# Kernel tuning notes

Measured on AMD Instinct MI355X. Metric: run time of the kernel, lower is better.

The kernel has to match this reference:

```python
import jax, jax.numpy as jnp
import numpy as np

NH = 8      # num_head
WIN = 7     # window
EPS = 1e-6


def _ln(x, w, b):
    m = x.mean(-1, keepdims=True)
    v = ((x - m) ** 2).mean(-1, keepdims=True)
    return (x - m) / jnp.sqrt(v + EPS) * w + b


def _dwconv(x, w, b):
    # x: [B,H,W,Cc], w: [7,7,1,Cc] (HWIO), depthwise (groups=Cc)
    y = jax.lax.conv_general_dilated(
        x, w, window_strides=(1, 1), padding='SAME',
        dimension_numbers=('NHWC', 'HWIO', 'NHWC'),
        feature_group_count=x.shape[-1])
    return y + b


def setup_inputs() -> dict:
    B, H, W, C = 16, 56, 56, 256
    RATIO = 8
    key = jax.random.key(0)
    ki = iter(jax.random.split(key, 48))
    def lin(i, o):
        return jax.random.normal(next(ki), (i, o), jnp.float32) * (1.0 / i) ** 0.5
    def bias(o):
        return jnp.zeros((o,), jnp.float32)
    def dw(c):
        return jax.random.normal(next(ki), (7, 7, 1, c), jnp.float32) * 0.05
    inp = {
        'x':   jax.random.normal(next(ki), (B, H, W, C), jnp.float32),
        'x_e': jax.random.normal(next(ki), (B, H, W, C // 2), jnp.float32),
        # LayerNorms
        'norm_w': jnp.ones((C,), jnp.float32),  'norm_b': bias(C),
        'norme_w': jnp.ones((C // 2,), jnp.float32), 'norme_b': bias(C // 2),
        # local_rr path
        'rr1_w': lin(C, C), 'rr1_b': bias(C),
        'rr2_w': lin(C, C), 'rr2_b': bias(C),
        'rr3_w': lin(C, C), 'rr3_b': bias(C),
        'conv_w': dw(C), 'conv_b': bias(C),
        # LocalAttentionRGBT
        'lx_l1_w': lin(C, C // 2), 'lx_l1_b': bias(C // 2),
        'lx_l2_w': lin(C // 2, C // 2), 'lx_l2_b': bias(C // 2),
        'lx_c1_w': dw(C // 2), 'lx_c1_b': bias(C // 2),
        'lx_c2_w': dw(C // 2), 'lx_c2_b': bias(C // 2),
        'lx_fc1_w': lin(C, C // RATIO),  # no bias
        'lx_fc2_w': lin(C // RATIO, C),  # no bias
        'lx_l3_w': lin(C, C // 2), 'lx_l3_b': bias(C // 2),
        # global pooled attention
        'kv_w': lin(C, C), 'kv_b': bias(C),
        'q_w': lin(C // 2 * 3, C // 2), 'q_b': bias(C // 2),
        # output projections (window != 0 => in = 2C)
        'proj_w': lin(2 * C, C), 'proj_b': bias(C),
        'proje_w': lin(2 * C, C // 2), 'proje_b': bias(C // 2),
    }
    return inp


def reference(x, x_e, norm_w, norm_b, norme_w, norme_b,
              rr1_w, rr1_b, rr2_w, rr2_b, rr3_w, rr3_b, conv_w, conv_b,
              lx_l1_w, lx_l1_b, lx_l2_w, lx_l2_b, lx_c1_w, lx_c1_b,
              lx_c2_w, lx_c2_b, lx_fc1_w, lx_fc2_w, lx_l3_w, lx_l3_b,
              kv_w, kv_b, q_w, q_b, proj_w, proj_b, proje_w, proje_b):
    B, H, W, C = x.shape
    hd = C // NH // 2  # head dim
    x = _ln(x, norm_w, norm_b)
    x_e = _ln(x_e, norme_w, norme_b)

    # --- local_rr: gated depthwise-conv branch ---
    rr1 = x @ rr1_w + rr1_b
    rr2 = _dwconv(x @ rr2_w + rr2_b, conv_w, conv_b)
    rr2 = rr2 @ rr3_w + rr3_b
    local_rr = rr1 * rr2  # [B,H,W,C]

    # --- LocalAttentionRGBT: cross-modal cosine-sim channel gate ---
    rgb = x @ lx_l1_w + lx_l1_b      # [B,H,W,C/2]
    t = x_e @ lx_l2_w + lx_l2_b      # [B,H,W,C/2]
    co = _dwconv(rgb * t, lx_c1_w, lx_c1_b)
    di = _dwconv(jnp.abs(rgb - t), lx_c2_w, lx_c2_b)
    co_di = jnp.concatenate([co, di], axis=-1)           # [B,H,W,C]
    amap = co_di.mean(-1, keepdims=True)                 # [B,H,W,1]
    dot = (amap * co_di).sum((1, 2), keepdims=True)      # [B,1,1,C]
    n1 = jnp.sqrt((amap ** 2).sum((1, 2), keepdims=True))
    n2 = jnp.sqrt((co_di ** 2).sum((1, 2), keepdims=True))
    cos_sim = dot / (n1 * n2 + 1e-6)                     # [B,1,1,C]
    attn_c = jax.nn.sigmoid(
        jax.nn.gelu(cos_sim @ lx_fc1_w, approximate=False) @ lx_fc2_w)
    local_rx = (co_di * attn_c) @ lx_l3_w + lx_l3_b      # [B,H,W,C/2]

    # --- global: pooled-q full-kv attention ---
    kv = (x @ kv_w + kv_b).reshape(B, H * W, 2, NH, hd).transpose(2, 0, 3, 1, 4)
    k, v = kv[0], kv[1]                                  # [B,NH,HW,hd]
    rx = jnp.concatenate([x, x_e], axis=-1)              # [B,H,W,3C/2]
    rx_pool = rx.reshape(B, WIN, H // WIN, WIN, W // WIN, -1).mean((2, 4))  # [B,7,7,3C/2]
    q = (rx_pool @ q_w + q_b).reshape(B, WIN * WIN, NH, hd).transpose(0, 2, 1, 3)
    scores = jnp.einsum('bnqd,bnkd->bnqk', q * hd ** -0.5, k)  # [B,NH,49,HW]
    attn = jax.nn.softmax(scores, axis=-1)
    g = jnp.einsum('bnqk,bnkd->bnqd', attn, v)           # [B,NH,49,hd]
    g = g.reshape(B, NH, WIN, WIN, hd).transpose(0, 1, 4, 2, 3).reshape(B, C // 2, WIN, WIN)
    g = jax.image.resize(g, (B, C // 2, H, W), method='bilinear')  # align_corners=False
    g = g.transpose(0, 2, 3, 1)                          # [B,H,W,C/2]

    cat = jnp.concatenate([local_rr, local_rx, g], axis=-1)  # [B,H,W,2C]
    x_e_out = cat @ proje_w + proje_b
    x_out = cat @ proj_w + proj_b
    return (x_out, x_e_out)
```

## Files before the change

### kernel.cpp

```cpp
#include <hip/hip_runtime.h>
#include <hip/hip_bf16.h>
#include <cstdint>
#include <cstddef>

#define N_TOK 50176
#define HWSZ  3136
#define BATCH 16

#define GF_MUL     1
#define GF_ASCALE  2
#define GF_KVSPLIT 4
#define GF_DUAL    8

typedef __hip_bfloat16 bf16;
typedef __attribute__((ext_vector_type(8))) short bf16x8;
typedef __attribute__((ext_vector_type(4))) float f32x4;
typedef __attribute__((ext_vector_type(4))) unsigned short u16x4;

__device__ __forceinline__ void  stf(float* p, size_t i, float v) { p[i] = v; }
__device__ __forceinline__ void  stf(bf16* p, size_t i, float v) { p[i] = __float2bfloat16(v); }
__device__ __forceinline__ float bu2f(unsigned short u) {
    unsigned int x = ((unsigned int)u) << 16; float f; __builtin_memcpy(&f, &x, 4); return f;
}
__device__ __forceinline__ unsigned short f2bu(float f) {
    bf16 t = __float2bfloat16(f); unsigned short u; __builtin_memcpy(&u, &t, 2); return u;
}

struct WtrDesc { const float* src; bf16* dst; int K; int N; int off; };
struct WtrPack { WtrDesc d[9]; int total; };
__global__ __launch_bounds__(256) void wtr_all(WtrPack p)
{
    int idx = blockIdx.x * 256 + threadIdx.x;
    if (idx >= p.total) return;
    #pragma unroll
    for (int s = 0; s < 9; s++) {
        int lo = p.d[s].off, hi = lo + p.d[s].K * p.d[s].N;
        if (idx >= lo && idx < hi) {
            int j = idx - lo;
            int k = j / p.d[s].N, n = j % p.d[s].N;
            p.d[s].dst[(size_t)n * p.d[s].K + k] = __float2bfloat16(p.d[s].src[j]);
        }
    }
}

__global__ __launch_bounds__(256) void ln_kernel(const float* __restrict__ in,
    const float* __restrict__ w, const float* __restrict__ b,
    bf16* __restrict__ out, int rows, int Cdim)
{
    int wave = threadIdx.x >> 6, lane = threadIdx.x & 63;
    int row = blockIdx.x * 4 + wave;
    if (row >= rows) return;
    const float* p = in + (size_t)row * Cdim;
    int nj = Cdim >> 6;
    float v[4];
    float s = 0.f;
    for (int j = 0; j < nj; j++) { v[j] = p[lane + 64 * j]; s += v[j]; }
    for (int off = 32; off; off >>= 1) s += __shfl_xor(s, off, 64);
    float mean = s / (float)Cdim;
    float vs = 0.f;
    for (int j = 0; j < nj; j++) { float d = v[j] - mean; vs += d * d; }
    for (int off = 32; off; off >>= 1) vs += __shfl_xor(vs, off, 64);
    float rstd = 1.f / sqrtf(vs / (float)Cdim + 1e-6f);
    bf16* q = out + (size_t)row * Cdim;
    for (int j = 0; j < nj; j++) {
        int c = lane + 64 * j;
        q[c] = __float2bfloat16((v[j] - mean) * rstd * w[c] + b[c]);
    }
}

#define LDT 40
template<int FLAGS, typename OT>
__global__ __launch_bounds__(256) void gemm_mfma(
    const bf16* __restrict__ A, int lda,
    const bf16* __restrict__ WT,
    const float* __restrict__ bias,
    OT* __restrict__ C, int ldc,
    int M, int K, int N,
    const bf16* __restrict__ mul, int mulld,
    const float* __restrict__ ascale,
    bf16* __restrict__ kout, bf16* __restrict__ vout,
    OT* __restrict__ C2, int ldc2, const float* __restrict__ bias2, int N1)
{
    __shared__ bf16 As[2][64][LDT];
    __shared__ bf16 Bs[2][128][LDT];
    int ntile = N >> 7;
    int bid = blockIdx.x;
    bid = (bid & 7) * (gridDim.x >> 3) + (bid >> 3);
    int m0 = (bid / ntile) * 64;
    int n0 = (bid % ntile) * 128;
    int tid = threadIdx.x;
    int lane = tid & 63, wid = tid >> 6;
    int wc = wid * 32;
    int lrow = lane & 15, lko = (lane >> 4) * 8;
    int sr = tid >> 2, sko = (tid & 3) * 8;

    f32x4 acc[4][2];
    #pragma unroll
    for (int i = 0; i < 4; i++)
        #pragma unroll
        for (int j = 0; j < 2; j++)
            acc[i][j] = (f32x4){0.f, 0.f, 0.f, 0.f};

#define GLOAD(RA, RB0, RB1, KOFF) do {                                                        \
    bf16x8 v_ = *reinterpret_cast<const bf16x8*>(A + (size_t)(m0 + sr) * lda + (KOFF) + sko); \
    if (FLAGS & GF_ASCALE) {                                                                  \
        int bidx_ = (m0 + sr) / HWSZ;                                                         \
        const float* as_ = ascale + (size_t)bidx_ * K + (KOFF) + sko;                         \
        for (int e_ = 0; e_ < 8; e_++)                                                        \
            v_[e_] = (short)f2bu(bu2f((unsigned short)v_[e_]) * as_[e_]);                     \
    }                                                                                         \
    RA = v_;                                                                                  \
    RB0 = *reinterpret_cast<const bf16x8*>(WT + (size_t)(n0 + sr) * K + (KOFF) + sko);        \
    RB1 = *reinterpret_cast<const bf16x8*>(WT + (size_t)(n0 + sr + 64) * K + (KOFF) + sko);   \
} while (0)

#define GWRITE(P, RA, RB0, RB1) do {                                   \
    *reinterpret_cast<bf16x8*>(&As[P][sr][sko]) = RA;                  \
    *reinterpret_cast<bf16x8*>(&Bs[P][sr][sko]) = RB0;                 \
    *reinterpret_cast<bf16x8*>(&Bs[P][sr + 64][sko]) = RB1;            \
} while (0)

#define GCOMP(P) do {                                                                         \
    bf16x8 af_[4], br_[2];                                                                    \
    for (int i_ = 0; i_ < 4; i_++)                                                            \
        af_[i_] = *reinterpret_cast<const bf16x8*>(&As[P][i_ * 16 + lrow][lko]);              \
    for (int j_ = 0; j_ < 2; j_++)                                                            \
        br_[j_] = *reinterpret_cast<const bf16x8*>(&Bs[P][wc + j_ * 16 + lrow][lko]);         \
    for (int i_ = 0; i_ < 4; i_++)                                                            \
        for (int j_ = 0; j_ < 2; j_++)                                                        \
            acc[i_][j_] = __builtin_amdgcn_mfma_f32_16x16x32_bf16(af_[i_], br_[j_], acc[i_][j_], 0, 0, 0); \
} while (0)

    bf16x8 ra0, rb00, rb01, ra1, rb10, rb11;
    GLOAD(ra0, rb00, rb01, 0);
    GLOAD(ra1, rb10, rb11, 32);
    int nst = K >> 5;
    for (int s = 0; s < nst; s += 2) {
        GWRITE(0, ra0, rb00, rb01);
        if (s + 2 < nst) GLOAD(ra0, rb00, rb01, (s + 2) * 32);
        __syncthreads();
        GCOMP(0);
        GWRITE(1, ra1, rb10, rb11);
        if (s + 3 < nst) GLOAD(ra1, rb10, rb11, (s + 3) * 32);
        __syncthreads();
        GCOMP(1);
    }
#undef GLOAD
#undef GWRITE
#undef GCOMP

    int orow = (lane >> 4) * 4;
    int ocol = lane & 15;
    #pragma unroll
    for (int i = 0; i < 4; i++) {
        #pragma unroll
        for (int j = 0; j < 2; j++) {
            #pragma unroll
            for (int p = 0; p < 4; p++) {
                int gm = m0 + i * 16 + orow + p;
                int gn = n0 + wc + j * 16 + ocol;
                if (FLAGS & GF_KVSPLIT) {
                    float v = acc[i][j][p] + bias[gn];
                    int bb = gm / HWSZ, n = gm % HWSZ;
                    if (gn < 128)
                        kout[(((size_t)bb * 8 + (gn >> 4)) * HWSZ + n) * 16 + (gn & 15)] = __float2bfloat16(v);
                    else {
                        int hh = (gn - 128) >> 4, dd = (gn - 128) & 15;
                        vout[(((size_t)bb * 8 + hh) * 16 + dd) * HWSZ + n] = __float2bfloat16(v);
                    }
                } else if (FLAGS & GF_DUAL) {
                    if (gn < N1) {
                        float v = acc[i][j][p] + bias[gn];
                        stf(C, (size_t)gm * ldc + gn, v);
                    } else {
                        float v = acc[i][j][p] + bias2[gn - N1];
                        stf(C2, (size_t)gm * ldc2 + (gn - N1), v);
                    }
                } else {
                    float v = acc[i][j][p] + bias[gn];
                    if (FLAGS & GF_MUL) v *= __bfloat162float(mul[(size_t)gm * mulld + gn]);
                    stf(C, (size_t)gm * ldc + gn, v);
                }
            }
        }
    }
}

__global__ __launch_bounds__(256) void gemm_k(
    const float* __restrict__ A, int lda,
    const float* __restrict__ Wt, const float* __restrict__ bias,
    float* __restrict__ Cc, int ldc, int M, int K, int Nc)
{
    __shared__ float As[16][68];
    __shared__ float Ws[16][64];
    int ntile = Nc >> 6;
    int tile_n = blockIdx.x % ntile;
    int tile_m = blockIdx.x / ntile;
    int m0 = tile_m * 64, n0 = tile_n * 64;
    int tid = threadIdx.x;
    int tx = tid & 15, ty = tid >> 4;
    float acc[4][4] = {};
    for (int k0 = 0; k0 < K; k0 += 16) {
        int ks = tid & 15, ms = tid >> 4;
        #pragma unroll
        for (int i = 0; i < 4; i++) {
            int gm = m0 + ms + i * 16;
            As[ks][ms + i * 16] = (gm < M) ? A[(size_t)gm * lda + k0 + ks] : 0.f;
        }
        #pragma unroll
        for (int j = 0; j < 4; j++) {
            int k = (tid >> 6) * 4 + j;
            Ws[k][tid & 63] = Wt[(size_t)(k0 + k) * Nc + n0 + (tid & 63)];
        }
        __syncthreads();
        #pragma unroll
        for (int k = 0; k < 16; k++) {
            float a[4], w[4];
            #pragma unroll
            for (int i = 0; i < 4; i++) a[i] = As[k][ty * 4 + i];
            #pragma unroll
            for (int j = 0; j < 4; j++) w[j] = Ws[k][tx * 4 + j];
            #pragma unroll
            for (int i = 0; i < 4; i++)
                #pragma unroll
                for (int j = 0; j < 4; j++)
                    acc[i][j] += a[i] * w[j];
        }
        __syncthreads();
    }
    #pragma unroll
    for (int i = 0; i < 4; i++) {
        int gm = m0 + ty * 4 + i;
        if (gm >= M) continue;
        #pragma unroll
        for (int j = 0; j < 4; j++) {
            int gn = n0 + tx * 4 + j;
            Cc[(size_t)gm * ldc + gn] = acc[i][j] + bias[gn];
        }
    }
}

__global__ __launch_bounds__(256) void dwconv_reg(const bf16* __restrict__ in,
    bf16* __restrict__ out,
    const float* __restrict__ w0, const float* __restrict__ b0,
    const float* __restrict__ w1, const float* __restrict__ b1, int split)
{
    int tid = threadIdx.x;
    int chg = tid & 31;
    int bsw = (blockIdx.x & 7) * 196 + (blockIdx.x >> 3);
    int pg  = bsw * 8 + (tid >> 5);
    int xg = pg % 14;
    int y  = (pg / 14) % 56;
    int b  = pg / (14 * 56);
    int c0 = chg * 8;
    int x0 = xg * 4;

    const float* wp; const float* bp; int ws, cw;
    if (c0 < split) { wp = w0; bp = b0; ws = split;       cw = c0; }
    else            { wp = w1; bp = b1; ws = 256 - split; cw = c0 - split; }

    float acc[4][8];
    #pragma unroll
    for (int o = 0; o < 4; o++)
        #pragma unroll
        for (int e = 0; e < 8; e++) acc[o][e] = 0.f;

    const bf16* base = in + (size_t)b * HWSZ * 256 + c0;
    const float* wbase = wp + cw;
    #pragma unroll
    for (int ky = 0; ky < 7; ky++) {
        int gy = y + ky - 3;
        if (gy < 0 || gy >= 56) continue;
        const bf16* rowp = base + (size_t)gy * 56 * 256;
        float cf[10][8];
        #pragma unroll
        for (int j = 0; j < 10; j++) {
            int gx = x0 + j - 3;
            bf16x8 v = {0, 0, 0, 0, 0, 0, 0, 0};
            if ((unsigned)gx < 56u)
                v = *reinterpret_cast<const bf16x8*>(rowp + (size_t)gx * 256);
            #pragma unroll
            for (int e = 0; e < 8; e++) cf[j][e] = bu2f((unsigned short)v[e]);
        }
        const float* wrow = wbase + ky * 7 * ws;
        #pragma unroll
        for (int kx = 0; kx < 7; kx++) {
            float4 wa = *reinterpret_cast<const float4*>(wrow + kx * ws);
            float4 wb = *reinterpret_cast<const float4*>(wrow + kx * ws + 4);
            #pragma unroll
            for (int o = 0; o < 4; o++) {
                acc[o][0] += cf[o + kx][0] * wa.x;
                acc[o][1] += cf[o + kx][1] * wa.y;
                acc[o][2] += cf[o + kx][2] * wa.z;
                acc[o][3] += cf[o + kx][3] * wa.w;
                acc[o][4] += cf[o + kx][4] * wb.x;
                acc[o][5] += cf[o + kx][5] * wb.y;
                acc[o][6] += cf[o + kx][6] * wb.z;
                acc[o][7] += cf[o + kx][7] * wb.w;
            }
        }
    }

    float4 ba = *reinterpret_cast<const float4*>(bp + cw);
    float4 bb = *reinterpret_cast<const float4*>(bp + cw + 4);
    bf16* obase = out + (((size_t)b * HWSZ + (size_t)y * 56 + x0) * 256) + c0;
    #pragma unroll
    for (int o = 0; o < 4; o++) {
        bf16x8 ov;
        ov[0] = (short)f2bu(acc[o][0] + ba.x);
        ov[1] = (short)f2bu(acc[o][1] + ba.y);
        ov[2] = (short)f2bu(acc[o][2] + ba.z);
        ov[3] = (short)f2bu(acc[o][3] + ba.w);
        ov[4] = (short)f2bu(acc[o][4] + bb.x);
        ov[5] = (short)f2bu(acc[o][5] + bb.y);
        ov[6] = (short)f2bu(acc[o][6] + bb.z);
        ov[7] = (short)f2bu(acc[o][7] + bb.w);
        *reinterpret_cast<bf16x8*>(obase + (size_t)o * 256) = ov;
    }
}

__global__ void rgbt_k(const bf16* __restrict__ rgb, const bf16* __restrict__ t,
                       bf16* __restrict__ codin, int total )
{
    int i = blockIdx.x * blockDim.x + threadIdx.x;
    if (i >= total) return;
    int n = i >> 7, c = i & 127;
    float a = __bfloat162float(rgb[i]), bb = __bfloat162float(t[i]);
    codin[(size_t)n * 256 + c] = __float2bfloat16(a * bb);
    codin[(size_t)n * 256 + 128 + c] = __float2bfloat16(fabsf(a - bb));
}

__global__ __launch_bounds__(256) void cosred_k(const bf16* __restrict__ codi,
    float* __restrict__ part)
{
    int b = blockIdx.x >> 4;
    int bi = blockIdx.x & 15;
    int wave = threadIdx.x >> 6, lane = threadIdx.x & 63;
    int slot = bi * 4 + wave;
    float dloc[4] = {0,0,0,0}, n2loc[4] = {0,0,0,0};
    float n1loc = 0.f;
    for (int i = 0; i < 49; i++) {
        int p = slot * 49 + i;
        const bf16* row = codi + ((size_t)b * HWSZ + p) * 256;
        float v[4]; float sum = 0.f;
        #pragma unroll
        for (int j = 0; j < 4; j++) { v[j] = __bfloat162float(row[lane + 64 * j]); sum += v[j]; }
        for (int off = 32; off; off >>= 1) sum += __shfl_xor(sum, off, 64);
        float amap = sum * (1.f / 256.f);
        #pragma unroll
        for (int j = 0; j < 4; j++) { dloc[j] += amap * v[j]; n2loc[j] += v[j] * v[j]; }
        n1loc += amap * amap;
    }
    float* dst = part + ((size_t)b * 64 + slot) * 513;
    #pragma unroll
    for (int j = 0; j < 4; j++) {
        dst[lane + 64 * j] = dloc[j];
        dst[256 + lane + 64 * j] = n2loc[j];
    }
    if (lane == 0) dst[512] = n1loc;
}

__global__ __launch_bounds__(256) void mlp_kernel(const float* __restrict__ part,
    const float* __restrict__ fc1w, const float* __restrict__ fc2w,
    float* __restrict__ attnc)
{
    int b = blockIdx.x;
    int tid = threadIdx.x;
    __shared__ float cosb[256];
    __shared__ float hbuf[32];
    const float* pb = part + (size_t)b * 64 * 513;
    float dot = 0.f, n2 = 0.f, n1 = 0.f;
    for (int s = 0; s < 64; s++) {
        dot += pb[s * 513 + tid];
        n2  += pb[s * 513 + 256 + tid];
        n1  += pb[s * 513 + 512];
    }
    float cs = dot / (sqrtf(n1) * sqrtf(n2) + 1e-6f);
    cosb[tid] = cs;
    __syncthreads();
    if (tid < 32) {
        float h = 0.f;
        for (int c = 0; c < 256; c++) h += cosb[c] * fc1w[c * 32 + tid];
        h = 0.5f * h * (1.f + erff(h * 0.70710678f));
        hbuf[tid] = h;
    }
    __syncthreads();
    float o = 0.f;
    for (int j = 0; j < 32; j++) o += hbuf[j] * fc2w[j * 256 + tid];
    attnc[b * 256 + tid] = 1.f / (1.f + expf(-o));
}

__global__ __launch_bounds__(384) void pool_kernel(const bf16* __restrict__ xn,
    const bf16* __restrict__ xen, float* __restrict__ rxpool)
{
    int bij = blockIdx.x;
    int b = bij / 49; int ij = bij % 49; int i = ij / 7, j = ij % 7;
    int c = threadIdx.x;
    float s = 0.f;
    for (int dy = 0; dy < 8; dy++)
        for (int dx = 0; dx < 8; dx++) {
            size_t n = ((size_t)b * 56 + (i * 8 + dy)) * 56 + (j * 8 + dx);
            s += (c < 256) ? __bfloat162float(xn[n * 256 + c])
                           : __bfloat162float(xen[n * 128 + (c - 256)]);
        }
    rxpool[(size_t)bij * 384 + c] = s * (1.f / 64.f);
}

#define NSPLIT 14
#define POSB   224
__global__ __launch_bounds__(256) void attn_mfma(const float* __restrict__ qbuf,
    const bf16* __restrict__ kbuf, const bf16* __restrict__ vtbuf,
    float* __restrict__ osplit, float* __restrict__ mlbuf)
{
    int bh = blockIdx.x & 127;
    int split = blockIdx.x >> 7;
    int b = bh >> 3, h = bh & 7;
    int tid = threadIdx.x;
    int qt = tid >> 6;
    int lane = tid & 63;
    int lo = lane & 15, hi = lane >> 4;

    bf16x8 qf = {0, 0, 0, 0, 0, 0, 0, 0};
    int q = qt * 16 + lo;
    if (hi < 2 && q < 49) {
        const float* qp = qbuf + ((size_t)b * 49 + q) * 128 + h * 16 + hi * 8;
        #pragma unroll
        for (int j = 0; j < 8; j++) qf[j] = (short)f2bu(qp[j] * 0.25f);
    }
    const bf16* kbase = kbuf + (size_t)bh * HWSZ * 16;
    const bf16* vbase = vtbuf + ((size_t)bh * 16 + lo) * HWSZ;

    float m_run = -1e30f, l_run = 0.f;
    f32x4 oacc = {0.f, 0.f, 0.f, 0.f};
    int pos1 = 8 * (lo >> 2) + (lo & 3);
    const f32x4 zz = {0.f, 0.f, 0.f, 0.f};

    for (int t = 0; t < POSB / 32; t++) {
        int base = split * POSB + t * 32;
        bf16x8 kf1 = {0, 0, 0, 0, 0, 0, 0, 0}, kf2 = kf1;
        if (hi < 2) {
            kf1 = *reinterpret_cast<const bf16x8*>(kbase + (size_t)(base + pos1) * 16 + hi * 8);
            kf2 = *reinterpret_cast<const bf16x8*>(kbase + (size_t)(base + pos1 + 4) * 16 + hi * 8);
        }
        bf16x8 vf = *reinterpret_cast<const bf16x8*>(vbase + base + hi * 8);
        f32x4 s1 = __builtin_amdgcn_mfma_f32_16x16x32_bf16(kf1, qf, zz, 0, 0, 0);
        f32x4 s2 = __builtin_amdgcn_mfma_f32_16x16x32_bf16(kf2, qf, zz, 0, 0, 0);
        float pmax = fmaxf(fmaxf(fmaxf(s1[0], s1[1]), fmaxf(s1[2], s1[3])),
                           fmaxf(fmaxf(s2[0], s2[1]), fmaxf(s2[2], s2[3])));
        pmax = fmaxf(pmax, __shfl_xor(pmax, 16, 64));
        pmax = fmaxf(pmax, __shfl_xor(pmax, 32, 64));
        float mnew = fmaxf(m_run, pmax);
        float esc = __expf(m_run - mnew);
        l_run *= esc;
        float e0 = __shfl(esc, 4 * hi + 0, 64);
        float e1 = __shfl(esc, 4 * hi + 1, 64);
        float e2 = __shfl(esc, 4 * hi + 2, 64);
        float e3 = __shfl(esc, 4 * hi + 3, 64);
        oacc[0] *= e0; oacc[1] *= e1; oacc[2] *= e2; oacc[3] *= e3;
        float p0 = __expf(s1[0] - mnew), p1 = __expf(s1[1] - mnew);
        float p2 = __expf(s1[2] - mnew), p3 = __expf(s1[3] - mnew);
        float p4 = __expf(s2[0] - mnew), p5 = __expf(s2[1] - mnew);
        float p6 = __expf(s2[2] - mnew), p7 = __expf(s2[3] - mnew);
        float rs = ((p0 + p1) + (p2 + p3)) + ((p4 + p5) + (p6 + p7));
        rs += __shfl_xor(rs, 16, 64);
        rs += __shfl_xor(rs, 32, 64);
        l_run += rs;
        m_run = mnew;
        bf16x8 pf;
        pf[0] = (short)f2bu(p0); pf[1] = (short)f2bu(p1);
        pf[2] = (short)f2bu(p2); pf[3] = (short)f2bu(p3);
        pf[4] = (short)f2bu(p4); pf[5] = (short)f2bu(p5);
        pf[6] = (short)f2bu(p6); pf[7] = (short)f2bu(p7);
        oacc = __builtin_amdgcn_mfma_f32_16x16x32_bf16(pf, vf, oacc, 0, 0, 0);
    }

    float* ob = osplit + ((size_t)bh * NSPLIT + split) * 64 * 16;
    #pragma unroll
    for (int r = 0; r < 4; r++) {
        int qq = qt * 16 + 4 * hi + r;
        ob[(size_t)qq * 16 + lo] = oacc[r];
    }
    if (hi == 0) {
        float* mlb = mlbuf + (((size_t)bh * NSPLIT + split) * 64 + qt * 16 + lo) * 2;
        mlb[0] = m_run; mlb[1] = l_run;
    }
}

__global__ __launch_bounds__(256) void attn_combine(const float* __restrict__ osplit,
    const float* __restrict__ mlbuf, float* __restrict__ gs)
{
    int idx = blockIdx.x * 256 + threadIdx.x;
    if (idx >= 128 * 49 * 16) return;
    int d = idx & 15;
    int pq = idx >> 4;
    int bh = pq / 49, q = pq % 49;
    float m[NSPLIT], l[NSPLIT];
    float M = -1e30f;
    #pragma unroll
    for (int s = 0; s < NSPLIT; s++) {
        const float* mlb = mlbuf + (((size_t)bh * NSPLIT + s) * 64 + q) * 2;
        m[s] = mlb[0]; l[s] = mlb[1];
        M = fmaxf(M, m[s]);
    }
    float L = 0.f, O = 0.f;
    #pragma unroll
    for (int s = 0; s < NSPLIT; s++) {
        float e = __expf(m[s] - M);
        L += l[s] * e;
        O += osplit[(((size_t)bh * NSPLIT + s) * 64 + q) * 16 + d] * e;
    }
    gs[(size_t)pq * 16 + d] = O / L;
}

__global__ void upsample_kernel(const float* __restrict__ gs, bf16* __restrict__ cat)
{
    int idx = blockIdx.x * blockDim.x + threadIdx.x;
    if (idx >= N_TOK * 128) return;
    int c = idx & 127;
    int pos = idx >> 7;
    int h = c >> 4, d = c & 15;
    int x = pos % 56;
    int y = (pos / 56) % 56;
    int b = pos / HWSZ;
    float sy = (y + 0.5f) * 0.125f - 0.5f;
    float sx = (x + 0.5f) * 0.125f - 0.5f;
    int y0f = (int)floorf(sy); float wy = sy - (float)y0f;
    int x0f = (int)floorf(sx); float wx = sx - (float)x0f;
    int y0 = max(0, min(6, y0f)), y1 = max(0, min(6, y0f + 1));
    int x0 = max(0, min(6, x0f)), x1 = max(0, min(6, x0f + 1));
    const float* g0 = gs + ((size_t)(b * 8 + h) * 49) * 16 + d;
    float v00 = g0[(y0 * 7 + x0) * 16], v01 = g0[(y0 * 7 + x1) * 16];
    float v10 = g0[(y1 * 7 + x0) * 16], v11 = g0[(y1 * 7 + x1) * 16];
    float v0 = v00 + (v01 - v00) * wx;
    float v1 = v10 + (v11 - v10) * wx;
    float v = v0 + (v1 - v0) * wy;
    cat[(size_t)pos * 512 + 384 + c] = __float2bfloat16(v);
}

extern "C" void kernel_launch(void* const* d_in, const int* in_sizes, int n_in,
                              void* d_out, int out_size, void* d_ws, size_t ws_size,
                              hipStream_t stream)
{
    const float* x      = (const float*)d_in[0];
    const float* x_e    = (const float*)d_in[1];
    const float* norm_w = (const float*)d_in[2];
    const float* norm_b = (const float*)d_in[3];
    const float* norme_w= (const float*)d_in[4];
    const float* norme_b= (const float*)d_in[5];
    const float* rr1_w  = (const float*)d_in[6];
    const float* rr1_b  = (const float*)d_in[7];
    const float* rr2_w  = (const float*)d_in[8];
    const float* rr2_b  = (const float*)d_in[9];
    const float* rr3_w  = (const float*)d_in[10];
    const float* rr3_b  = (const float*)d_in[11];
    const float* conv_w = (const float*)d_in[12];
    const float* conv_b = (const float*)d_in[13];
    const float* l1_w   = (const float*)d_in[14];
    const float* l1_b   = (const float*)d_in[15];
    const float* l2_w   = (const float*)d_in[16];
    const float* l2_b   = (const float*)d_in[17];
    const float* c1_w   = (const float*)d_in[18];
    const float* c1_b   = (const float*)d_in[19];
    const float* c2_w   = (const float*)d_in[20];
    const float* c2_b   = (const float*)d_in[21];
    const float* fc1_w  = (const float*)d_in[22];
    const float* fc2_w  = (const float*)d_in[23];
    const float* l3_w   = (const float*)d_in[24];
    const float* l3_b   = (const float*)d_in[25];
    const float* kv_w   = (const float*)d_in[26];
    const float* kv_b   = (const float*)d_in[27];
    const float* q_w    = (const float*)d_in[28];
    const float* q_b    = (const float*)d_in[29];
    const float* proj_w = (const float*)d_in[30];
    const float* proj_b = (const float*)d_in[31];
    const float* proje_w= (const float*)d_in[32];
    const float* proje_b= (const float*)d_in[33];

    float* part   = (float*)d_ws;
    float* attnc  = part   + (size_t)525312;
    float* gs     = attnc  + 4096;
    float* rxpool = gs     + 100352;
    float* qbuf   = rxpool + 301056;
    bf16* wt      = (bf16*)(qbuf + 100352);
    bf16* rr1_t  = wt;
    bf16* rr2_t  = rr1_t + 65536;
    bf16* rr3_t  = rr2_t + 65536;
    bf16* kv_t   = rr3_t + 65536;
    bf16* l1_t   = kv_t  + 65536;
    bf16* l2_t   = l1_t  + 32768;
    bf16* l3_t   = l2_t  + 16384;
    bf16* proj_t = l3_t  + 32768;
    bf16* proje_t= proj_t + 131072;
    bf16* xn     = proje_t + 65536;
    bf16* xen    = xn   + (size_t)N_TOK * 256;
    bf16* bufC   = xen  + (size_t)N_TOK * 128;
    bf16* bufD   = bufC + (size_t)N_TOK * 256;
    bf16* bufE   = bufD + (size_t)N_TOK * 256;
    bf16* cat    = bufE + (size_t)N_TOK * 256;
    size_t need = (size_t)((char*)(cat + (size_t)N_TOK * 512) - (char*)d_ws);
    if (ws_size < need) return;

    bf16* kbuf = bufC;
    bf16* vbuf = bufC + (size_t)N_TOK * 128;

    float* osplit = (float*)bufD;
    float* mlbuf  = osplit + (size_t)128 * NSPLIT * 64 * 16;

    float* xout  = (float*)d_out;
    float* xeout = xout + (size_t)N_TOK * 256;

    const int nthr = 256;
    auto mgrid = [](int M, int N) { return dim3((M / 64) * (N / 128)); };

    {
        WtrPack p;
        const float* srcs[9] = {rr1_w, rr2_w, rr3_w, kv_w, l1_w, l2_w, l3_w, proj_w, proje_w};
        bf16* dsts[9] = {rr1_t, rr2_t, rr3_t, kv_t, l1_t, l2_t, l3_t, proj_t, proje_t};
        int Ks[9] = {256, 256, 256, 256, 256, 128, 256, 512, 512};
        int Ns[9] = {256, 256, 256, 256, 128, 128, 128, 256, 128};
        int off = 0;
        for (int s = 0; s < 9; s++) {
            p.d[s] = {srcs[s], dsts[s], Ks[s], Ns[s], off};
            off += Ks[s] * Ns[s];
        }
        p.total = off;
        wtr_all<<<dim3((off + 255) / 256), dim3(256), 0, stream>>>(p);
    }

    ln_kernel<<<dim3(N_TOK / 4), dim3(nthr), 0, stream>>>(x, norm_w, norm_b, xn, N_TOK, 256);
    ln_kernel<<<dim3(N_TOK / 4), dim3(nthr), 0, stream>>>(x_e, norme_w, norme_b, xen, N_TOK, 128);

    gemm_mfma<GF_DUAL, bf16><<<mgrid(N_TOK, 512), dim3(nthr), 0, stream>>>(
        xn, 256, rr1_t, rr1_b, bufC, 256, N_TOK, 256, 512, nullptr, 0, nullptr, nullptr, nullptr,
        bufD, 256, rr2_b, 256);
    dwconv_reg<<<dim3(N_TOK / 32), dim3(nthr), 0, stream>>>(
        bufD, bufE, conv_w, conv_b, conv_w, conv_b, 256);
    gemm_mfma<GF_MUL, bf16><<<mgrid(N_TOK, 256), dim3(nthr), 0, stream>>>(
        bufE, 256, rr3_t, rr3_b, cat, 512, N_TOK, 256, 256, bufC, 256, nullptr, nullptr, nullptr,
        nullptr, 0, nullptr, 0);

    gemm_mfma<0, bf16><<<mgrid(N_TOK, 128), dim3(nthr), 0, stream>>>(
        xn, 256, l1_t, l1_b, bufD, 128, N_TOK, 256, 128, nullptr, 0, nullptr, nullptr, nullptr,
        nullptr, 0, nullptr, 0);
    gemm_mfma<0, bf16><<<mgrid(N_TOK, 128), dim3(nthr), 0, stream>>>(
        xen, 128, l2_t, l2_b, bufD + (size_t)N_TOK * 128, 128, N_TOK, 128, 128, nullptr, 0, nullptr, nullptr, nullptr,
        nullptr, 0, nullptr, 0);
    rgbt_k<<<dim3((N_TOK * 128) / nthr), dim3(nthr), 0, stream>>>(
        bufD, bufD + (size_t)N_TOK * 128, bufC, N_TOK * 128);
    dwconv_reg<<<dim3(N_TOK / 32), dim3(nthr), 0, stream>>>(
        bufC, bufE, c1_w, c1_b, c2_w, c2_b, 128);
    cosred_k<<<dim3(BATCH * 16), dim3(nthr), 0, stream>>>(bufE, part);
    mlp_kernel<<<dim3(BATCH), dim3(nthr), 0, stream>>>(part, fc1_w, fc2_w, attnc);
    gemm_mfma<GF_ASCALE, bf16><<<mgrid(N_TOK, 128), dim3(nthr), 0, stream>>>(
        bufE, 256, l3_t, l3_b, cat + 256, 512, N_TOK, 256, 128, nullptr, 0, attnc, nullptr, nullptr,
        nullptr, 0, nullptr, 0);

    gemm_mfma<GF_KVSPLIT, bf16><<<mgrid(N_TOK, 256), dim3(nthr), 0, stream>>>(
        xn, 256, kv_t, kv_b, (bf16*)nullptr, 0, N_TOK, 256, 256, nullptr, 0, nullptr, kbuf, vbuf,
        nullptr, 0, nullptr, 0);
    pool_kernel<<<dim3(BATCH * 49), dim3(384), 0, stream>>>(xn, xen, rxpool);
    gemm_k<<<dim3(((784 + 63) / 64) * 2), dim3(nthr), 0, stream>>>(
        rxpool, 384, q_w, q_b, qbuf, 128, 784, 384, 128);
    attn_mfma<<<dim3(128 * NSPLIT), dim3(nthr), 0, stream>>>(qbuf, kbuf, vbuf, osplit, mlbuf);
    attn_combine<<<dim3(392), dim3(nthr), 0, stream>>>(osplit, mlbuf, gs);
    upsample_kernel<<<dim3((N_TOK * 128) / nthr), dim3(nthr), 0, stream>>>(gs, cat);

    gemm_mfma<GF_DUAL, float><<<mgrid(N_TOK, 384), dim3(nthr), 0, stream>>>(
        cat, 512, proj_t, proj_b, xout, 256, N_TOK, 512, 384, nullptr, 0, nullptr, nullptr, nullptr,
        xeout, 128, proje_b, 256);
}
```

Measured before the change: 428.1 us.

## Fuse KV projection into rr1/rr2 GEMM and fold rgbt into l2 GEMM epilogue

Reorders the transposed weights so rr1, rr2 and kv sit contiguously, which lets one GEMM with N=768 compute all three projections of the normalized x. That GEMM writes the kv output directly into a new dedicated K/V buffer, so xn is read once instead of twice. Separately, the l2 GEMM epilogue now computes the product and absolute difference with the l1 output, which removes the rgbt_k kernel and its intermediate round trip. The cost is extra workspace for the separate kv buffer and a more branchy epilogue.

```diff
diff --git a/kernel.cpp b/kernel.cpp
--- a/kernel.cpp
+++ b/kernel.cpp
@@ -11,6 +11,8 @@
 #define GF_ASCALE  2
 #define GF_KVSPLIT 4
 #define GF_DUAL    8
+#define GF_TRI     16
+#define GF_RGBT    32
 
 typedef __hip_bfloat16 bf16;
 typedef __attribute__((ext_vector_type(8))) short bf16x8;
@@ -159,7 +161,28 @@
             for (int p = 0; p < 4; p++) {
                 int gm = m0 + i * 16 + orow + p;
                 int gn = n0 + wc + j * 16 + ocol;
-                if (FLAGS & GF_KVSPLIT) {
+                if (FLAGS & GF_TRI) {
+                    if (gn < 256) {
+                        stf(C, (size_t)gm * ldc + gn, acc[i][j][p] + bias[gn]);
+                    } else if (gn < 512) {
+                        stf(C2, (size_t)gm * ldc2 + (gn - 256), acc[i][j][p] + bias2[gn - 256]);
+                    } else {
+                        int g3 = gn - 512;
+                        float v = acc[i][j][p] + ascale[g3];
+                        int bb = gm / HWSZ, n = gm % HWSZ;
+                        if (g3 < 128)
+                            kout[(((size_t)bb * 8 + (g3 >> 4)) * HWSZ + n) * 16 + (g3 & 15)] = __float2bfloat16(v);
+                        else {
+                            int hh = (g3 - 128) >> 4, dd = (g3 - 128) & 15;
+                            vout[(((size_t)bb * 8 + hh) * 16 + dd) * HWSZ + n] = __float2bfloat16(v);
+                        }
+                    }
+                } else if (FLAGS & GF_RGBT) {
+                    float t = acc[i][j][p] + bias[gn];
+                    float rgb = __bfloat162float(mul[(size_t)gm * mulld + gn]);
+                    stf(C, (size_t)gm * ldc + gn, rgb * t);
+                    stf(C, (size_t)gm * ldc + 128 + gn, fabsf(rgb - t));
+                } else if (FLAGS & GF_KVSPLIT) {
                     float v = acc[i][j][p] + bias[gn];
                     int bb = gm / HWSZ, n = gm % HWSZ;
                     if (gn < 128)
@@ -317,17 +340,6 @@
         ov[7] = (short)f2bu(acc[o][7] + bb.w);
         *reinterpret_cast<bf16x8*>(obase + (size_t)o * 256) = ov;
     }
-}
-
-__global__ void rgbt_k(const bf16* __restrict__ rgb, const bf16* __restrict__ t,
-                       bf16* __restrict__ codin, int total )
-{
-    int i = blockIdx.x * blockDim.x + threadIdx.x;
-    if (i >= total) return;
-    int n = i >> 7, c = i & 127;
-    float a = __bfloat162float(rgb[i]), bb = __bfloat162float(t[i]);
-    codin[(size_t)n * 256 + c] = __float2bfloat16(a * bb);
-    codin[(size_t)n * 256 + 128 + c] = __float2bfloat16(fabsf(a - bb));
 }
 
 __global__ __launch_bounds__(256) void cosred_k(const bf16* __restrict__ codi,
@@ -584,9 +596,9 @@
     bf16* wt      = (bf16*)(qbuf + 100352);
     bf16* rr1_t  = wt;
     bf16* rr2_t  = rr1_t + 65536;
-    bf16* rr3_t  = rr2_t + 65536;
-    bf16* kv_t   = rr3_t + 65536;
-    bf16* l1_t   = kv_t  + 65536;
+    bf16* kv_t   = rr2_t + 65536;
+    bf16* rr3_t  = kv_t  + 65536;
+    bf16* l1_t   = rr3_t + 65536;
     bf16* l2_t   = l1_t  + 32768;
     bf16* l3_t   = l2_t  + 16384;
     bf16* proj_t = l3_t  + 32768;
@@ -597,11 +609,12 @@
     bf16* bufD   = bufC + (size_t)N_TOK * 256;
     bf16* bufE   = bufD + (size_t)N_TOK * 256;
     bf16* cat    = bufE + (size_t)N_TOK * 256;
-    size_t need = (size_t)((char*)(cat + (size_t)N_TOK * 512) - (char*)d_ws);
+    bf16* kvbuf  = cat  + (size_t)N_TOK * 512;
+    size_t need = (size_t)((char*)(kvbuf + (size_t)N_TOK * 256) - (char*)d_ws);
     if (ws_size < need) return;
 
-    bf16* kbuf = bufC;
-    bf16* vbuf = bufC + (size_t)N_TOK * 128;
+    bf16* kbuf = kvbuf;
+    bf16* vbuf = kvbuf + (size_t)N_TOK * 128;
 
     float* osplit = (float*)bufD;
     float* mlbuf  = osplit + (size_t)128 * NSPLIT * 64 * 16;
@@ -614,8 +627,8 @@
 
     {
         WtrPack p;
-        const float* srcs[9] = {rr1_w, rr2_w, rr3_w, kv_w, l1_w, l2_w, l3_w, proj_w, proje_w};
-        bf16* dsts[9] = {rr1_t, rr2_t, rr3_t, kv_t, l1_t, l2_t, l3_t, proj_t, proje_t};
+        const float* srcs[9] = {rr1_w, rr2_w, kv_w, rr3_w, l1_w, l2_w, l3_w, proj_w, proje_w};
+        bf16* dsts[9] = {rr1_t, rr2_t, kv_t, rr3_t, l1_t, l2_t, l3_t, proj_t, proje_t};
         int Ks[9] = {256, 256, 256, 256, 256, 128, 256, 512, 512};
         int Ns[9] = {256, 256, 256, 256, 128, 128, 128, 256, 128};
         int off = 0;
@@ -630,9 +643,9 @@
     ln_kernel<<<dim3(N_TOK / 4), dim3(nthr), 0, stream>>>(x, norm_w, norm_b, xn, N_TOK, 256);
     ln_kernel<<<dim3(N_TOK / 4), dim3(nthr), 0, stream>>>(x_e, norme_w, norme_b, xen, N_TOK, 128);
 
-    gemm_mfma<GF_DUAL, bf16><<<mgrid(N_TOK, 512), dim3(nthr), 0, stream>>>(
-        xn, 256, rr1_t, rr1_b, bufC, 256, N_TOK, 256, 512, nullptr, 0, nullptr, nullptr, nullptr,
-        bufD, 256, rr2_b, 256);
+    gemm_mfma<GF_TRI, bf16><<<mgrid(N_TOK, 768), dim3(nthr), 0, stream>>>(
+        xn, 256, rr1_t, rr1_b, bufC, 256, N_TOK, 256, 768, nullptr, 0, kv_b, kbuf, vbuf,
+        bufD, 256, rr2_b, 0);
     dwconv_reg<<<dim3(N_TOK / 32), dim3(nthr), 0, stream>>>(
         bufD, bufE, conv_w, conv_b, conv_w, conv_b, 256);
     gemm_mfma<GF_MUL, bf16><<<mgrid(N_TOK, 256), dim3(nthr), 0, stream>>>(
@@ -642,11 +655,9 @@
     gemm_mfma<0, bf16><<<mgrid(N_TOK, 128), dim3(nthr), 0, stream>>>(
         xn, 256, l1_t, l1_b, bufD, 128, N_TOK, 256, 128, nullptr, 0, nullptr, nullptr, nullptr,
         nullptr, 0, nullptr, 0);
-    gemm_mfma<0, bf16><<<mgrid(N_TOK, 128), dim3(nthr), 0, stream>>>(
-        xen, 128, l2_t, l2_b, bufD + (size_t)N_TOK * 128, 128, N_TOK, 128, 128, nullptr, 0, nullptr, nullptr, nullptr,
+    gemm_mfma<GF_RGBT, bf16><<<mgrid(N_TOK, 128), dim3(nthr), 0, stream>>>(
+        xen, 128, l2_t, l2_b, bufC, 256, N_TOK, 128, 128, bufD, 128, nullptr, nullptr, nullptr,
         nullptr, 0, nullptr, 0);
-    rgbt_k<<<dim3((N_TOK * 128) / nthr), dim3(nthr), 0, stream>>>(
-        bufD, bufD + (size_t)N_TOK * 128, bufC, N_TOK * 128);
     dwconv_reg<<<dim3(N_TOK / 32), dim3(nthr), 0, stream>>>(
         bufC, bufE, c1_w, c1_b, c2_w, c2_b, 128);
     cosred_k<<<dim3(BATCH * 16), dim3(nthr), 0, stream>>>(bufE, part);
@@ -655,9 +666,6 @@
         bufE, 256, l3_t, l3_b, cat + 256, 512, N_TOK, 256, 128, nullptr, 0, attnc, nullptr, nullptr,
         nullptr, 0, nullptr, 0);
 
-    gemm_mfma<GF_KVSPLIT, bf16><<<mgrid(N_TOK, 256), dim3(nthr), 0, stream>>>(
-        xn, 256, kv_t, kv_b, (bf16*)nullptr, 0, N_TOK, 256, 256, nullptr, 0, nullptr, kbuf, vbuf,
-        nullptr, 0, nullptr, 0);
     pool_kernel<<<dim3(BATCH * 49), dim3(384), 0, stream>>>(xn, xen, rxpool);
     gemm_k<<<dim3(((784 + 63) / 64) * 2), dim3(nthr), 0, stream>>>(
         rxpool, 384, q_w, q_b, qbuf, 128, 784, 384, 128);
```

Result: no change. 423.4 us (median of 2 runs) (-1.1%).
